# Optimization experiments

Hardware: AMD Instinct MI355X
Metric: run time of the kernel (lower is better)

The kernel has to match this reference:

```python
import jax, jax.numpy as jnp
import numpy as np

N_TOKENS = 32768
HIDDEN = 2048
NUM_EXPERTS = 64
TOP_K = 2


def setup_inputs() -> dict:
    key = jax.random.key(0)
    kx, kw = jax.random.split(key)
    x = jax.random.normal(kx, (N_TOKENS, HIDDEN), dtype=jnp.float32)
    # nn.Linear weight init scale ~ 1/sqrt(fan_in)
    gate_w = jax.random.normal(kw, (HIDDEN, NUM_EXPERTS), dtype=jnp.float32) / np.sqrt(HIDDEN)
    return {"x": x, "gate_w": gate_w}


def reference(x, gate_w):
    # logits: [N, E]
    logits = x @ gate_w
    # top-k over experts
    top_k_logits, top_k_indices = jax.lax.top_k(logits, TOP_K)  # [N, K]
    top_k_weights = jax.nn.softmax(top_k_logits, axis=-1)        # [N, K]
    probs = jax.nn.softmax(logits, axis=-1)                      # [N, E]
    # per-expert routed-token counts via segment-sum over flattened top-k indices
    tokens_per_expert = jax.ops.segment_sum(
        jnp.ones((x.shape[0] * TOP_K,), dtype=x.dtype),
        top_k_indices.reshape(-1),
        num_segments=NUM_EXPERTS,
    )
    f = tokens_per_expert / max(x.shape[0], 1)   # fraction of tokens per expert
    P = probs.mean(axis=0)                        # mean router prob per expert
    load_balance_loss = NUM_EXPERTS * jnp.sum(f * P)
    return top_k_weights, top_k_indices, load_balance_loss
```

## Files before the change

### kernel.cpp

```cpp
#include <hip/hip_runtime.h>
#include <math.h>

#define N_TOKENS 32768
#define HIDDEN   2048
#define NEXP     64
#define BM 32
#define NWAVE 4
#define NBLK (N_TOKENS / BM)
#define KSTEP 32
#define NSTEP 16
#define XSCALE 64.f
#define WSCALE 256.f
#define DESCALE (1.f / 16384.f)
#define NG 64

typedef __attribute__((ext_vector_type(8))) _Float16 half8;
typedef __attribute__((ext_vector_type(4))) float f32x4;

__global__ void wsplit_kernel(const float* __restrict__ gw,
                              _Float16* __restrict__ wh, _Float16* __restrict__ wl) {
    __shared__ float tile[KSTEP * NEXP];
    const int S   = blockIdx.x;
    const int tid = threadIdx.x;
    const float4* g4 = reinterpret_cast<const float4*>(gw + (size_t)S * KSTEP * NEXP);
    float4* t4 = reinterpret_cast<float4*>(tile);
    t4[tid]       = g4[tid];
    t4[tid + 256] = g4[tid + 256];
    __syncthreads();
    const int nt  = tid >> 6;
    const int l   = tid & 63;
    const int col = nt * 16 + (l & 15);
    const int kr  = (l >> 4) * 8;
    half8 vh, vl;
    #pragma unroll
    for (int j = 0; j < 8; ++j) {
        const float w = tile[(kr + j) * NEXP + col] * WSCALE;
        const _Float16 hh = (_Float16)w;
        vh[j] = hh;
        vl[j] = (_Float16)(w - (float)hh);
    }
    const size_t off = ((size_t)(S * 4 + nt) * 64 + l) * 8;
    *reinterpret_cast<half8*>(wh + off) = vh;
    *reinterpret_cast<half8*>(wl + off) = vl;
}

__global__ __launch_bounds__(256, 4)
void router_main(const float* __restrict__ x,
                 const _Float16* __restrict__ whp, const _Float16* __restrict__ wlp,
                 float* __restrict__ out_w, float* __restrict__ out_i,
                 float* __restrict__ wsP, int* __restrict__ wsC)
{
    __shared__ float part[NWAVE][BM][65];
    __shared__ float pred[NWAVE][NEXP];
    __shared__ int   cntl[NEXP];

    const int tid  = threadIdx.x;
    const int lane = tid & 63;
    const int wv   = tid >> 6;
    const int m0   = blockIdx.x * BM;
    if (tid < NEXP) cntl[tid] = 0;

    const int mrow = lane & 15;
    const int kq   = lane >> 4;
    const int Sb   = wv * NSTEP;

    const float* xb = x + (size_t)(m0 + mrow) * HIDDEN + (size_t)wv * 512 + kq * 8;

    f32x4 a[2][2][2];
    half8 bh[4], bl[4];
    f32x4 acc[2][4];
    const f32x4 zero = {0.f, 0.f, 0.f, 0.f};
    #pragma unroll
    for (int mt = 0; mt < 2; ++mt)
        #pragma unroll
        for (int nt = 0; nt < 4; ++nt) acc[mt][nt] = zero;

    #define LOADA(SET, s_) {                                                          \
        _Pragma("unroll")                                                             \
        for (int mt = 0; mt < 2; ++mt) {                                              \
            const float* g_ = xb + (size_t)mt * (16 * HIDDEN) + (s_) * KSTEP;         \
            a[SET][mt][0] = *reinterpret_cast<const f32x4*>(g_);                      \
            a[SET][mt][1] = *reinterpret_cast<const f32x4*>(g_ + 4);                  \
        } }
    #define LOADB(s_) {                                                               \
        const int S_ = Sb + (s_);                                                     \
        _Pragma("unroll")                                                             \
        for (int nt = 0; nt < 4; ++nt) {                                              \
            const size_t o_ = ((size_t)(S_ * 4 + nt) * 64 + lane) * 8;                \
            bh[nt] = *reinterpret_cast<const half8*>(whp + o_);                       \
            bl[nt] = *reinterpret_cast<const half8*>(wlp + o_);                       \
        } }
    #define COMPUTE(AS) {                                                             \
        half8 ah[2], al[2];                                                           \
        _Pragma("unroll")                                                             \
        for (int mt = 0; mt < 2; ++mt)                                                \
            _Pragma("unroll")                                                         \
            for (int h = 0; h < 2; ++h)                                               \
                _Pragma("unroll")                                                     \
                for (int j = 0; j < 4; ++j) {                                         \
                    const float v_ = a[AS][mt][h][j] * XSCALE;                        \
                    const _Float16 hh_ = (_Float16)v_;                                \
                    ah[mt][h * 4 + j] = hh_;                                          \
                    al[mt][h * 4 + j] = (_Float16)(v_ - (float)hh_);                  \
                }                                                                     \
        _Pragma("unroll")                                                             \
        for (int mt = 0; mt < 2; ++mt)                                                \
            _Pragma("unroll")                                                         \
            for (int nt = 0; nt < 4; ++nt) {                                          \
                f32x4 c_ = acc[mt][nt];                                               \
                c_ = __builtin_amdgcn_mfma_f32_16x16x32_f16(ah[mt], bh[nt], c_, 0, 0, 0); \
                c_ = __builtin_amdgcn_mfma_f32_16x16x32_f16(ah[mt], bl[nt], c_, 0, 0, 0); \
                c_ = __builtin_amdgcn_mfma_f32_16x16x32_f16(al[mt], bh[nt], c_, 0, 0, 0); \
                acc[mt][nt] = c_;                                                     \
            } }

    LOADA(0, 0); LOADB(0);

    for (int t = 0; t < NSTEP / 2; ++t) {
        const int s = t * 2;
        LOADA(1, s + 1);
        COMPUTE(0);
        LOADB(s + 1);
        if (s + 2 < NSTEP) LOADA(0, s + 2);
        COMPUTE(1);
        if (s + 2 < NSTEP) LOADB(s + 2);
    }
    #undef LOADA
    #undef LOADB
    #undef COMPUTE

    #pragma unroll
    for (int mt = 0; mt < 2; ++mt)
        #pragma unroll
        for (int nt = 0; nt < 4; ++nt)
            #pragma unroll
            for (int r = 0; r < 4; ++r)
                part[wv][mt * 16 + (lane >> 4) * 4 + r][nt * 16 + (lane & 15)] =
                    acc[mt][nt][r] * DESCALE;
    __syncthreads();

    float sumP = 0.f;
    for (int t = 0; t < BM / NWAVE; ++t) {
        const int m = wv * (BM / NWAVE) + t;
        const float l = part[0][m][lane] + part[1][m][lane]
                      + part[2][m][lane] + part[3][m][lane];

        float v = l; int idx = lane;
        #pragma unroll
        for (int off = 32; off >= 1; off >>= 1) {
            float ov = __shfl_xor(v, off);
            int   oi = __shfl_xor(idx, off);
            if (ov > v || (ov == v && oi < idx)) { v = ov; idx = oi; }
        }
        const float v1 = v; const int i1 = idx;
        v = (lane == i1) ? -INFINITY : l;
        idx = lane;
        #pragma unroll
        for (int off = 32; off >= 1; off >>= 1) {
            float ov = __shfl_xor(v, off);
            int   oi = __shfl_xor(idx, off);
            if (ov > v || (ov == v && oi < idx)) { v = ov; idx = oi; }
        }
        const float v2 = v; const int i2 = idx;
        const float ed  = expf(v2 - v1);
        const float wt1 = 1.f / (1.f + ed);
        const float wt2 = ed / (1.f + ed);
        const float p = expf(l - v1);
        float Z = p;
        #pragma unroll
        for (int off = 32; off >= 1; off >>= 1) Z += __shfl_xor(Z, off);
        sumP += p / Z;
        if (lane == 0) {
            const size_t o = (size_t)(m0 + m) * 2;
            out_w[o]     = wt1;
            out_w[o + 1] = wt2;
            out_i[o]     = (float)i1;
            out_i[o + 1] = (float)i2;
            atomicAdd(&cntl[i1], 1);
            atomicAdd(&cntl[i2], 1);
        }
    }
    pred[wv][lane] = sumP;
    __syncthreads();
    if (tid < NEXP) {
        float s = 0.f;
        #pragma unroll
        for (int w2 = 0; w2 < NWAVE; ++w2) s += pred[w2][tid];
        wsP[(size_t)blockIdx.x * NEXP + tid] = s;
        wsC[(size_t)blockIdx.x * NEXP + tid] = cntl[tid];
    }
}

__global__ void router_fin1(const float* __restrict__ wsP, const int* __restrict__ wsC,
                            float* __restrict__ Ps1, float* __restrict__ Cs1)
{
    const int g = blockIdx.x;
    const int e = threadIdx.x;
    float P = 0.f, C = 0.f;
    #pragma unroll
    for (int r = 0; r < NBLK / NG; ++r) {
        const size_t row = (size_t)(g * (NBLK / NG) + r) * NEXP + e;
        P += wsP[row];
        C += (float)wsC[row];
    }
    Ps1[(size_t)g * NEXP + e] = P;
    Cs1[(size_t)g * NEXP + e] = C;
}

__global__ void router_fin2(const float* __restrict__ Ps1, const float* __restrict__ Cs1,
                            float* __restrict__ out_loss)
{
    const int e = threadIdx.x;
    float P = 0.f, C = 0.f;
    #pragma unroll
    for (int g = 0; g < NG; ++g) {
        P += Ps1[(size_t)g * NEXP + e];
        C += Cs1[(size_t)g * NEXP + e];
    }
    float val = (C / (float)N_TOKENS) * (P / (float)N_TOKENS);
    #pragma unroll
    for (int off = 32; off >= 1; off >>= 1) val += __shfl_xor(val, off);
    if (e == 0) out_loss[0] = (float)NEXP * val;
}

extern "C" void kernel_launch(void* const* d_in, const int* in_sizes, int n_in,
                              void* d_out, int out_size, void* d_ws, size_t ws_size,
                              hipStream_t stream) {
    const float* x  = (const float*)d_in[0];
    const float* gw = (const float*)d_in[1];
    float* out   = (float*)d_out;
    float* out_w = out;
    float* out_i = out + (size_t)N_TOKENS * 2;
    float* loss  = out + (size_t)N_TOKENS * 4;
    float*    wsP = (float*)d_ws;
    int*      wsC = (int*)((char*)d_ws + 262144);
    _Float16* wh  = (_Float16*)((char*)d_ws + 524288);
    _Float16* wl  = wh + (size_t)HIDDEN * NEXP;
    float*    Ps1 = (float*)((char*)d_ws + 1048576);
    float*    Cs1 = Ps1 + NG * NEXP;
    hipLaunchKernelGGL(wsplit_kernel, dim3(HIDDEN / KSTEP), dim3(256), 0, stream, gw, wh, wl);
    hipLaunchKernelGGL(router_main, dim3(NBLK), dim3(256), 0, stream,
                       x, wh, wl, out_w, out_i, wsP, wsC);
    hipLaunchKernelGGL(router_fin1, dim3(NG), dim3(64), 0, stream, wsP, wsC, Ps1, Cs1);
    hipLaunchKernelGGL(router_fin2, dim3(1), dim3(64), 0, stream, Ps1, Cs1, loss);
}
```

Measured before the change: 82.29 us.

## Stage x tiles via global_load_lds into swizzled LDS double buffer

New measurement: 97.79 us. 18.8% more time.

```diff
diff --git a/kernel.cpp b/kernel.cpp
--- a/kernel.cpp
+++ b/kernel.cpp
@@ -17,6 +17,12 @@
 typedef __attribute__((ext_vector_type(8))) _Float16 half8;
 typedef __attribute__((ext_vector_type(4))) float f32x4;
 
+__device__ __forceinline__ void gload16(const void* g, void* l) {
+    __builtin_amdgcn_global_load_lds(
+        (const __attribute__((address_space(1))) void*)g,
+        (__attribute__((address_space(3))) void*)l, 16, 0, 0);
+}
+
 __global__ void wsplit_kernel(const float* __restrict__ gw,
                               _Float16* __restrict__ wh, _Float16* __restrict__ wl) {
     __shared__ float tile[KSTEP * NEXP];
@@ -50,7 +56,7 @@
                  float* __restrict__ out_w, float* __restrict__ out_i,
                  float* __restrict__ wsP, int* __restrict__ wsC)
 {
-    __shared__ float part[NWAVE][BM][65];
+    __shared__ __align__(16) float arena[8320];
     __shared__ float pred[NWAVE][NEXP];
     __shared__ int   cntl[NEXP];
 
@@ -60,13 +66,15 @@
     const int m0   = blockIdx.x * BM;
     if (tid < NEXP) cntl[tid] = 0;
 
-    const int mrow = lane & 15;
-    const int kq   = lane >> 4;
     const int Sb   = wv * NSTEP;
-
-    const float* xb = x + (size_t)(m0 + mrow) * HIDDEN + (size_t)wv * 512 + kq * 8;
-
-    f32x4 a[2][2][2];
+    const int wvK  = wv * 512;
+    const int wvA  = wv * 1024;
+
+    const int stok = lane >> 3;
+    const int su   = (lane & 7) ^ stok;
+    const int t7   = lane & 7;
+    const int vb   = (lane >> 4) * 2;
+
     half8 bh[4], bl[4];
     f32x4 acc[2][4];
     const f32x4 zero = {0.f, 0.f, 0.f, 0.f};
@@ -75,12 +83,12 @@
         #pragma unroll
         for (int nt = 0; nt < 4; ++nt) acc[mt][nt] = zero;
 
-    #define LOADA(SET, s_) {                                                          \
-        _Pragma("unroll")                                                             \
-        for (int mt = 0; mt < 2; ++mt) {                                              \
-            const float* g_ = xb + (size_t)mt * (16 * HIDDEN) + (s_) * KSTEP;         \
-            a[SET][mt][0] = *reinterpret_cast<const f32x4*>(g_);                      \
-            a[SET][mt][1] = *reinterpret_cast<const f32x4*>(g_ + 4);                  \
+    #define STAGEA(s_, buf_) {                                                        \
+        const int k0_ = wvK + (s_) * KSTEP;                                           \
+        _Pragma("unroll")                                                             \
+        for (int i = 0; i < 4; ++i) {                                                 \
+            const float* g_ = x + (size_t)(m0 + i * 8 + stok) * HIDDEN + k0_ + su * 4;\
+            gload16(g_, arena + (buf_) * 4096 + wvA + i * 256);                       \
         } }
     #define LOADB(s_) {                                                               \
         const int S_ = Sb + (s_);                                                     \
@@ -90,60 +98,79 @@
             bh[nt] = *reinterpret_cast<const half8*>(whp + o_);                       \
             bl[nt] = *reinterpret_cast<const half8*>(wlp + o_);                       \
         } }
-    #define COMPUTE(AS) {                                                             \
-        half8 ah[2], al[2];                                                           \
+    #define BODY(s_, VMC, DO_STAGE, DO_LOADB) {                                       \
+        asm volatile("s_waitcnt vmcnt(" #VMC ")" ::: "memory");                       \
+        __builtin_amdgcn_sched_barrier(0);                                            \
+        const float* abase_ = arena + ((s_) & 1) * 4096 + wvA;                        \
+        f32x4 q_[2][2];                                                               \
+        _Pragma("unroll")                                                             \
+        for (int mt = 0; mt < 2; ++mt) {                                              \
+            const float* xrow_ = abase_ + (mt * 16 + (lane & 15)) * 32;               \
+            q_[mt][0] = *reinterpret_cast<const f32x4*>(xrow_ + ((vb ^ t7) << 2));    \
+            q_[mt][1] = *reinterpret_cast<const f32x4*>(xrow_ + (((vb + 1) ^ t7) << 2)); \
+        }                                                                             \
+        asm volatile("s_waitcnt lgkmcnt(0)" ::: "memory");                            \
+        __builtin_amdgcn_sched_barrier(0);                                            \
+        if (DO_STAGE) STAGEA((s_) + 2, (s_) & 1);                                     \
+        half8 ah_[2], al_[2];                                                         \
         _Pragma("unroll")                                                             \
         for (int mt = 0; mt < 2; ++mt)                                                \
             _Pragma("unroll")                                                         \
             for (int h = 0; h < 2; ++h)                                               \
                 _Pragma("unroll")                                                     \
                 for (int j = 0; j < 4; ++j) {                                         \
-                    const float v_ = a[AS][mt][h][j] * XSCALE;                        \
+                    const float v_ = q_[mt][h][j] * XSCALE;                           \
                     const _Float16 hh_ = (_Float16)v_;                                \
-                    ah[mt][h * 4 + j] = hh_;                                          \
-                    al[mt][h * 4 + j] = (_Float16)(v_ - (float)hh_);                  \
+                    ah_[mt][h * 4 + j] = hh_;                                         \
+                    al_[mt][h * 4 + j] = (_Float16)(v_ - (float)hh_);                 \
                 }                                                                     \
         _Pragma("unroll")                                                             \
         for (int mt = 0; mt < 2; ++mt)                                                \
             _Pragma("unroll")                                                         \
             for (int nt = 0; nt < 4; ++nt) {                                          \
                 f32x4 c_ = acc[mt][nt];                                               \
-                c_ = __builtin_amdgcn_mfma_f32_16x16x32_f16(ah[mt], bh[nt], c_, 0, 0, 0); \
-                c_ = __builtin_amdgcn_mfma_f32_16x16x32_f16(ah[mt], bl[nt], c_, 0, 0, 0); \
-                c_ = __builtin_amdgcn_mfma_f32_16x16x32_f16(al[mt], bh[nt], c_, 0, 0, 0); \
+                c_ = __builtin_amdgcn_mfma_f32_16x16x32_f16(ah_[mt], bh[nt], c_, 0, 0, 0); \
+                c_ = __builtin_amdgcn_mfma_f32_16x16x32_f16(ah_[mt], bl[nt], c_, 0, 0, 0); \
+                c_ = __builtin_amdgcn_mfma_f32_16x16x32_f16(al_[mt], bh[nt], c_, 0, 0, 0); \
                 acc[mt][nt] = c_;                                                     \
-            } }
-
-    LOADA(0, 0); LOADB(0);
-
-    for (int t = 0; t < NSTEP / 2; ++t) {
-        const int s = t * 2;
-        LOADA(1, s + 1);
-        COMPUTE(0);
-        LOADB(s + 1);
-        if (s + 2 < NSTEP) LOADA(0, s + 2);
-        COMPUTE(1);
-        if (s + 2 < NSTEP) LOADB(s + 2);
-    }
-    #undef LOADA
+            }                                                                         \
+        if (DO_LOADB) LOADB((s_) + 1);                                                \
+    }
+
+    STAGEA(0, 0); STAGEA(1, 1); LOADB(0);
+
+    BODY(0, 12, 1, 1);
+    for (int t = 0; t < 7; ++t) {
+        const int s = 1 + t * 2;
+        BODY(s, 20, 1, 1);
+        BODY(s + 1, 20, (s + 1) < 14, 1);
+    }
+    BODY(15, 16, 0, 0);
+    #undef STAGEA
     #undef LOADB
-    #undef COMPUTE
-
-    #pragma unroll
-    for (int mt = 0; mt < 2; ++mt)
-        #pragma unroll
-        for (int nt = 0; nt < 4; ++nt)
+    #undef BODY
+
+    __syncthreads();
+    {
+        float* part = arena + wv * (BM * 65);
+        #pragma unroll
+        for (int mt = 0; mt < 2; ++mt)
             #pragma unroll
-            for (int r = 0; r < 4; ++r)
-                part[wv][mt * 16 + (lane >> 4) * 4 + r][nt * 16 + (lane & 15)] =
-                    acc[mt][nt][r] * DESCALE;
+            for (int nt = 0; nt < 4; ++nt)
+                #pragma unroll
+                for (int r = 0; r < 4; ++r)
+                    part[(mt * 16 + (lane >> 4) * 4 + r) * 65 + nt * 16 + (lane & 15)] =
+                        acc[mt][nt][r] * DESCALE;
+    }
     __syncthreads();
 
     float sumP = 0.f;
     for (int t = 0; t < BM / NWAVE; ++t) {
         const int m = wv * (BM / NWAVE) + t;
-        const float l = part[0][m][lane] + part[1][m][lane]
-                      + part[2][m][lane] + part[3][m][lane];
+        const float l = arena[0 * (BM * 65) + m * 65 + lane]
+                      + arena[1 * (BM * 65) + m * 65 + lane]
+                      + arena[2 * (BM * 65) + m * 65 + lane]
+                      + arena[3 * (BM * 65) + m * 65 + lane];
 
         float v = l; int idx = lane;
         #pragma unroll
```
